# Kernel tuning notes

Measured on AMD Instinct MI355X. Metric: run time of the kernel, lower is better.

Reference implementation:

```python
import jax, jax.numpy as jnp
import numpy as np

B, S, D, H = 4, 2048, 1024, 16
HD = D // H


def setup_inputs() -> dict:
    key = jax.random.key(0)
    ks = jax.random.split(key, 9)
    s = 0.02  # GPT-2 init scale for weights
    return {
        "hidden_states": jax.random.normal(ks[0], (B, S, D), jnp.float32),
        "Wq": jax.random.normal(ks[1], (D, D), jnp.float32) * s,
        "bq": jnp.zeros((D,), jnp.float32),
        "Wk": jax.random.normal(ks[2], (D, D), jnp.float32) * s,
        "bk": jnp.zeros((D,), jnp.float32),
        "Wv": jax.random.normal(ks[3], (D, D), jnp.float32) * s,
        "bv": jnp.zeros((D,), jnp.float32),
        "Wo": jax.random.normal(ks[4], (D, D), jnp.float32) * s,
        "bo": jnp.zeros((D,), jnp.float32),
    }


def _split_heads(x):
    b, s, _ = x.shape
    return x.reshape(b, s, H, HD).transpose(0, 2, 1, 3)  # [B,H,S,HD]


def reference(hidden_states, Wq, bq, Wk, bk, Wv, bv, Wo, bo):
    b, s, d = hidden_states.shape
    q = _split_heads(hidden_states @ Wq + bq)
    k = _split_heads(hidden_states @ Wk + bk)
    v = _split_heads(hidden_states @ Wv + bv)
    # naive attention: full [B,H,S,S] scores, scale, causal where-mask, softmax, AV
    scores = jnp.einsum('bhqd,bhkd->bhqk', q, k)
    scores = scores / jnp.asarray(HD, scores.dtype) ** 0.5  # scale_attn_weights
    causal = jnp.tril(jnp.ones((s, s), dtype=bool))  # bias buffer slice
    scores = jnp.where(causal, scores, jnp.finfo(scores.dtype).min)
    attn = jax.nn.softmax(scores, axis=-1)  # attn_dropout p=0 -> identity
    out = jnp.einsum('bhqk,bhkd->bhqd', attn, v)
    out = out.transpose(0, 2, 1, 3).reshape(b, s, d)  # merge heads
    return out @ Wo + bo  # resid_dropout p=0 -> identity
```

## Files before the change

### kernel.cpp

```cpp
#include <hip/hip_runtime.h>
#include <stdint.h>


#define GAS __attribute__((address_space(1)))
#define LAS __attribute__((address_space(3)))

typedef __attribute__((ext_vector_type(4))) float f32x4;
typedef __attribute__((ext_vector_type(8))) short bf16x8;

__device__ __forceinline__ short f2bf(float f) {
  union { float f; uint32_t u; } v; v.f = f;
  uint32_t r = v.u + 0x7fffu + ((v.u >> 16) & 1u);
  return (short)(r >> 16);
}

__device__ __forceinline__ float bf2f(short s) {
  union { uint32_t u; float f; } v;
  v.u = ((uint32_t)(uint16_t)s) << 16;
  return v.f;
}

__device__ __forceinline__ uint32_t cvt_pk_bf16(float lo, float hi) {
  uint32_t r;
  asm("v_cvt_pk_bf16_f32 %0, %1, %2" : "=v"(r) : "v"(lo), "v"(hi));
  return r;
}

__device__ __forceinline__ void gload_lds16(const void* g, void* l) {
  __builtin_amdgcn_global_load_lds((const GAS void*)g, (LAS void*)l, 16, 0, 0);
}

#define GATE(N)                                            \
  __builtin_amdgcn_sched_barrier(0);                       \
  asm volatile("s_waitcnt vmcnt(" #N ")" ::: "memory");    \
  __builtin_amdgcn_s_barrier();                            \
  __builtin_amdgcn_sched_barrier(0);

#define BAR_LGKM                                           \
  __builtin_amdgcn_sched_barrier(0);                       \
  asm volatile("s_waitcnt lgkmcnt(0)" ::: "memory");       \
  __builtin_amdgcn_s_barrier();                            \
  __builtin_amdgcn_sched_barrier(0);

__global__ __launch_bounds__(256) void cvt_bf16_kernel(const float* __restrict__ in,
                                                       short* __restrict__ out, int n4) {
  int i = blockIdx.x * blockDim.x + threadIdx.x;
  int stride = gridDim.x * blockDim.x;
  for (int idx = i; idx < n4; idx += stride) {
    float4 v = ((const float4*)in)[idx];
    short4 o;
    o.x = f2bf(v.x); o.y = f2bf(v.y); o.z = f2bf(v.z); o.w = f2bf(v.w);
    ((short4*)out)[idx] = o;
  }
}

__global__ __launch_bounds__(256) void wt4_kernel(const float* __restrict__ W0,
                                                  const float* __restrict__ W1,
                                                  const float* __restrict__ W2,
                                                  const float* __restrict__ W3,
                                                  short* __restrict__ Wt) {
  __shared__ short tile[64][65];
  const float* W = (blockIdx.z == 0) ? W0 : (blockIdx.z == 1) ? W1
                   : (blockIdx.z == 2) ? W2 : W3;
  short* dst = Wt + ((size_t)blockIdx.z << 20);
  const int k0 = blockIdx.x * 64, n0 = blockIdx.y * 64;
  const int t = threadIdx.x;
#pragma unroll
  for (int i = 0; i < 16; ++i) {
    int r = (t >> 6) + i * 4, c = t & 63;
    tile[r][c] = f2bf(W[(size_t)(k0 + r) * 1024 + n0 + c]);
  }
  __syncthreads();
#pragma unroll
  for (int i = 0; i < 16; ++i) {
    int r = (t >> 6) + i * 4, c = t & 63;
    dst[(size_t)(n0 + r) * 1024 + k0 + c] = tile[c][r];
  }
}

template <int MODE>
__global__ __launch_bounds__(512, 2) void gemm2(const short* __restrict__ A,
                                                const short* __restrict__ Bt,
                                                const float* __restrict__ b0,
                                                const float* __restrict__ b1,
                                                const float* __restrict__ b2,
                                                void* __restrict__ O0,
                                                void* __restrict__ O1,
                                                void* __restrict__ O2) {
  __shared__ short lds[4][12288];
  const int xcd = (int)blockIdx.x & 7;
  const int t = (int)blockIdx.x >> 3;
  const int m0 = (xcd * 4 + (t & 3)) * 256;
  const int n0 = (t >> 2) * 128;
  const int tid = threadIdx.x;
  const int lane = tid & 63, w = tid >> 6;
  const int l15 = lane & 15, lg = lane >> 4;
  const int wm = w >> 1, wn = w & 1;

  const short* ag[2];
  const short* bg;
#pragma unroll
  for (int i = 0; i < 2; ++i) {
    const int P = w * 64 + i * 512 + lane;
    const int L = P ^ ((P >> 3) & 7);
    ag[i] = A + (size_t)(m0 + (L >> 2)) * 1024 + (L & 3) * 8;
  }
  {
    const int P = w * 64 + lane;
    const int L = P ^ ((P >> 3) & 7);
    bg = Bt + (size_t)(n0 + (L >> 2)) * 1024 + (L & 3) * 8;
  }

  int aof[4], bof[4];
#pragma unroll
  for (int mf = 0; mf < 4; ++mf) {
    const int L = (wm * 64 + mf * 16 + l15) * 4 + lg;
    aof[mf] = (L ^ ((L >> 3) & 7)) * 8;
  }
#pragma unroll
  for (int nf = 0; nf < 4; ++nf) {
    const int L = (wn * 64 + nf * 16 + l15) * 4 + lg;
    bof[nf] = (L ^ ((L >> 3) & 7)) * 8;
  }

  f32x4 acc[4][4];
#pragma unroll
  for (int i = 0; i < 4; ++i)
#pragma unroll
    for (int j = 0; j < 4; ++j) acc[i][j] = (f32x4){0.f, 0.f, 0.f, 0.f};

  auto stage = [&](int bi, int kt) {
    short* As = &lds[bi][0];
    short* Bs = &lds[bi][8192];
#pragma unroll
    for (int i = 0; i < 2; ++i)
      gload_lds16(ag[i] + kt * 32, As + (w * 64 + i * 512) * 8);
    gload_lds16(bg + kt * 32, Bs + (w * 64) * 8);
  };

  auto compute = [&](int bi) {
    const short* As = &lds[bi][0];
    const short* Bs = &lds[bi][8192];
    bf16x8 a[4], b[4];
#pragma unroll
    for (int mf = 0; mf < 4; ++mf) a[mf] = *(const bf16x8*)&As[aof[mf]];
#pragma unroll
    for (int nf = 0; nf < 4; ++nf) b[nf] = *(const bf16x8*)&Bs[bof[nf]];
    __builtin_amdgcn_s_setprio(1);
#pragma unroll
    for (int mf = 0; mf < 4; ++mf)
#pragma unroll
      for (int nf = 0; nf < 4; ++nf)
        acc[mf][nf] =
            __builtin_amdgcn_mfma_f32_16x16x32_bf16(a[mf], b[nf], acc[mf][nf], 0, 0, 0);
    __builtin_amdgcn_s_setprio(0);
  };

  stage(0, 0);
  stage(1, 1);
  stage(2, 2);

  for (int j = 0; j < 29; ++j) {
    GATE(6)
    stage((j + 3) & 3, j + 3);
    compute(j & 3);
  }
  GATE(6) compute(1);
  GATE(3) compute(2);
  GATE(0) compute(3);

  if (MODE == 1) {
    float* dst = (float*)O0;
#pragma unroll
    for (int mf = 0; mf < 4; ++mf)
#pragma unroll
      for (int nf = 0; nf < 4; ++nf) {
        const int col = n0 + wn * 64 + nf * 16 + l15;
        const float bv = b0[col];
#pragma unroll
        for (int rr = 0; rr < 4; ++rr) {
          const int row = m0 + wm * 64 + mf * 16 + lg * 4 + rr;
          dst[(size_t)row * 1024 + col] = acc[mf][nf][rr] + bv;
        }
      }
  } else {
    const int mat = n0 >> 10;
    const int nc0 = n0 & 1023;
    const float* bias = (mat == 0) ? b0 : (mat == 1) ? b1 : b2;
    if (mat < 2) {
      short* dst = (short*)(mat == 0 ? O0 : O1);
#pragma unroll
      for (int mf = 0; mf < 4; ++mf)
#pragma unroll
        for (int nf = 0; nf < 4; ++nf) {
          const int col = nc0 + wn * 64 + nf * 16 + l15;
          const float bv = bias[col];
          const int h = col >> 6, hd = col & 63;
#pragma unroll
          for (int rr = 0; rr < 4; ++rr) {
            const int row = m0 + wm * 64 + mf * 16 + lg * 4 + rr;
            const int b = row >> 11, s = row & 2047;
            dst[((size_t)(b * 16 + h) * 2048 + s) * 64 + hd] = f2bf(acc[mf][nf][rr] + bv);
          }
        }
    } else {
      short* dst = (short*)O2;
#pragma unroll
      for (int mf = 0; mf < 4; ++mf) {
        const int rowb = m0 + wm * 64 + mf * 16 + lg * 4;
        const int b = rowb >> 11, s = rowb & 2047;
#pragma unroll
        for (int nf = 0; nf < 4; ++nf) {
          const int col = nc0 + wn * 64 + nf * 16 + l15;
          const float bv = bias[col];
          const int h = col >> 6, hd = col & 63;
          short4 sv;
          sv.x = f2bf(acc[mf][nf][0] + bv);
          sv.y = f2bf(acc[mf][nf][1] + bv);
          sv.z = f2bf(acc[mf][nf][2] + bv);
          sv.w = f2bf(acc[mf][nf][3] + bv);
          *(short4*)&dst[((size_t)(b * 16 + h) * 64 + hd) * 2048 + s] = sv;
        }
      }
    }
  }
}

__global__ __launch_bounds__(256) void attn_kernel(const short* __restrict__ Q,
                                                   const short* __restrict__ K,
                                                   const short* __restrict__ Vt,
                                                   short* __restrict__ Oout) {
  __shared__ short Ks[2][4096];
  __shared__ short Vs[2][4096];
  const int bh = blockIdx.x;
  const int jq = 15 - (int)blockIdx.y;
  const int q0 = jq * 128;
  const int tid = threadIdx.x;
  const int lane = tid & 63, w = tid >> 6;
  const int l15 = lane & 15, lg = lane >> 4;
  const short* Qb = Q + (size_t)bh * 2048 * 64;
  const short* Kb = K + (size_t)bh * 2048 * 64;
  const short* Vb = Vt + (size_t)bh * 64 * 2048;
  const int b = bh >> 4, h = bh & 15;
  const float SC = 0.18033688011112042f;
  const int qg0 = q0 + w * 32;

  bf16x8 qf[2][2];
#pragma unroll
  for (int qs = 0; qs < 2; ++qs)
#pragma unroll
    for (int kk = 0; kk < 2; ++kk) {
      bf16x8 rq =
          *(const bf16x8*)&Qb[(size_t)(qg0 + qs * 16 + l15) * 64 + kk * 32 + lg * 8];
      union { uint32_t u[4]; bf16x8 v; } sq;
#pragma unroll
      for (int d = 0; d < 4; ++d)
        sq.u[d] = cvt_pk_bf16(bf2f(rq[2 * d]) * SC, bf2f(rq[2 * d + 1]) * SC);
      qf[qs][kk] = sq.v;
    }

  const short* kg[2];
  const short* vg[2];
#pragma unroll
  for (int i = 0; i < 2; ++i) {
    const int P = (w * 2 + i) * 64 + lane;
    const int L = P ^ ((P >> 3) & 7);
    kg[i] = Kb + (size_t)(L >> 3) * 64 + (L & 7) * 8;
    vg[i] = Vb + (size_t)(L >> 3) * 2048 + (L & 7) * 8;
  }

  int kcol[2], vca[2], vcb[2];
#pragma unroll
  for (int kk = 0; kk < 2; ++kk) {
    kcol[kk] = (((kk * 4 + lg) ^ (l15 & 7)) << 3);
    vca[kk] = (((kk * 4 + (lg >> 1)) ^ (l15 & 7)) << 3) + (lg & 1) * 4;
    vcb[kk] = (((kk * 4 + 2 + (lg >> 1)) ^ (l15 & 7)) << 3) + (lg & 1) * 4;
  }

  f32x4 o[2][4];
#pragma unroll
  for (int i = 0; i < 2; ++i)
#pragma unroll
    for (int j = 0; j < 4; ++j) o[i][j] = (f32x4){0.f, 0.f, 0.f, 0.f};
  f32x4 psum[2] = {(f32x4){0.f, 0.f, 0.f, 0.f}, (f32x4){0.f, 0.f, 0.f, 0.f}};

  const int nkt = 2 * jq + 2;
#pragma unroll
  for (int i = 0; i < 2; ++i) {
    gload_lds16(kg[i], &Ks[0][(w * 2 + i) * 512]);
    gload_lds16(vg[i], &Vs[0][(w * 2 + i) * 512]);
  }

  int cur = 0;
  for (int kt = 0; kt < nkt; ++kt) {
    if (kt + 1 < nkt) {
#pragma unroll
      for (int i = 0; i < 2; ++i) {
        gload_lds16(kg[i] + (kt + 1) * 4096, &Ks[cur ^ 1][(w * 2 + i) * 512]);
        gload_lds16(vg[i] + (kt + 1) * 64, &Vs[cur ^ 1][(w * 2 + i) * 512]);
      }
      GATE(4)
    } else {
      GATE(0)
    }

    if (kt * 64 <= qg0 + 31) {
      const short* Kc = &Ks[cur][0];
      const short* Vc = &Vs[cur][0];

      f32x4 sacc[4][2];
#pragma unroll
      for (int t = 0; t < 4; ++t)
#pragma unroll
        for (int qs = 0; qs < 2; ++qs) sacc[t][qs] = (f32x4){0.f, 0.f, 0.f, 0.f};
      __builtin_amdgcn_s_setprio(1);
#pragma unroll
      for (int t = 0; t < 4; ++t) {
        const int krow = (t * 16 + l15) * 64;
#pragma unroll
        for (int kk = 0; kk < 2; ++kk) {
          bf16x8 kf = *(const bf16x8*)&Kc[krow + kcol[kk]];
#pragma unroll
          for (int qs = 0; qs < 2; ++qs)
            sacc[t][qs] = __builtin_amdgcn_mfma_f32_16x16x32_bf16(kf, qf[qs][kk],
                                                                  sacc[t][qs], 0, 0, 0);
        }
      }
      __builtin_amdgcn_s_setprio(0);

      if (kt * 64 + 63 > qg0) {
#pragma unroll
        for (int t = 0; t < 4; ++t)
#pragma unroll
          for (int qs = 0; qs < 2; ++qs)
#pragma unroll
            for (int r = 0; r < 4; ++r) {
              const int kg_ = kt * 64 + t * 16 + lg * 4 + r;
              const int qg = qg0 + qs * 16 + l15;
              if (kg_ > qg) sacc[t][qs][r] = -3e38f;
            }
      }

      bf16x8 pa[2][2];
#pragma unroll
      for (int qs = 0; qs < 2; ++qs) {
#pragma unroll
        for (int t = 0; t < 4; ++t)
#pragma unroll
          for (int r = 0; r < 4; ++r) {
            const float p = __builtin_amdgcn_exp2f(sacc[t][qs][r]);
            sacc[t][qs][r] = p;
            psum[qs][r] += p;
          }
#pragma unroll
        for (int kk = 0; kk < 2; ++kk) {
          union { uint32_t u[4]; bf16x8 v; } pw;
          pw.u[0] = cvt_pk_bf16(sacc[2 * kk][qs][0], sacc[2 * kk][qs][1]);
          pw.u[1] = cvt_pk_bf16(sacc[2 * kk][qs][2], sacc[2 * kk][qs][3]);
          pw.u[2] = cvt_pk_bf16(sacc[2 * kk + 1][qs][0], sacc[2 * kk + 1][qs][1]);
          pw.u[3] = cvt_pk_bf16(sacc[2 * kk + 1][qs][2], sacc[2 * kk + 1][qs][3]);
          pa[qs][kk] = pw.v;
        }
      }

      __builtin_amdgcn_s_setprio(1);
#pragma unroll
      for (int ds = 0; ds < 4; ++ds) {
        const int vrow = (ds * 16 + l15) * 64;
#pragma unroll
        for (int kk = 0; kk < 2; ++kk) {
          union { short s[8]; bf16x8 v; short4 h2[2]; } vu;
          vu.h2[0] = *(const short4*)&Vc[vrow + vca[kk]];
          vu.h2[1] = *(const short4*)&Vc[vrow + vcb[kk]];
#pragma unroll
          for (int qs = 0; qs < 2; ++qs)
            o[qs][ds] = __builtin_amdgcn_mfma_f32_16x16x32_bf16(pa[qs][kk], vu.v,
                                                                o[qs][ds], 0, 0, 0);
        }
      }
      __builtin_amdgcn_s_setprio(0);
    }

    BAR_LGKM
    cur ^= 1;
  }

#pragma unroll
  for (int qs = 0; qs < 2; ++qs) {
    float s = psum[qs][0] + psum[qs][1] + psum[qs][2] + psum[qs][3];
    s += __shfl_xor(s, 16);
    s += __shfl_xor(s, 32);
    psum[qs][0] = 1.f / s;
  }

#pragma unroll
  for (int qs = 0; qs < 2; ++qs) {
    float on[4];
#pragma unroll
    for (int r = 0; r < 4; ++r)
      on[r] = __shfl(psum[qs][0], (lane & 48) | (lg * 4 + r));
#pragma unroll
    for (int ds = 0; ds < 4; ++ds)
#pragma unroll
      for (int r = 0; r < 4; ++r) {
        const int qg = q0 + w * 32 + qs * 16 + lg * 4 + r;
        const int col = h * 64 + ds * 16 + l15;
        Oout[((size_t)(b * 2048 + qg)) * 1024 + col] = f2bf(o[qs][ds][r] * on[r]);
      }
  }
}

extern "C" void kernel_launch(void* const* d_in, const int* in_sizes, int n_in,
                              void* d_out, int out_size, void* d_ws, size_t ws_size,
                              hipStream_t stream) {
  const float* hs = (const float*)d_in[0];
  const float* Wq = (const float*)d_in[1];
  const float* bq = (const float*)d_in[2];
  const float* Wk = (const float*)d_in[3];
  const float* bk = (const float*)d_in[4];
  const float* Wv = (const float*)d_in[5];
  const float* bv = (const float*)d_in[6];
  const float* Wo = (const float*)d_in[7];
  const float* bo = (const float*)d_in[8];

  char* ws = (char*)d_ws;
  short* Xbf = (short*)(ws + 0);
  short* Qb  = (short*)(ws + ((size_t)16 << 20));
  short* Kb  = (short*)(ws + ((size_t)32 << 20));
  short* Vtb = (short*)(ws + ((size_t)48 << 20));
  short* Wts = (short*)(ws + ((size_t)64 << 20));
  short* Wot = Wts + ((size_t)3 << 20);

  cvt_bf16_kernel<<<2048, 256, 0, stream>>>(hs, Xbf, (8192 * 1024) / 4);
  wt4_kernel<<<dim3(16, 16, 4), 256, 0, stream>>>(Wq, Wk, Wv, Wo, Wts);

  gemm2<0><<<768, 512, 0, stream>>>(Xbf, Wts, bq, bk, bv, Qb, Kb, Vtb);

  attn_kernel<<<dim3(64, 16), 256, 0, stream>>>(Qb, Kb, Vtb, Xbf);

  gemm2<1><<<256, 512, 0, stream>>>(Xbf, Wot, bo, nullptr, nullptr,
                                    (float*)d_out, nullptr, nullptr);
}
```

Baseline: 159.0 us.

## Triple-buffer KV in attention, permute V layout, compute row sums via MFMA

```diff
diff --git a/kernel.cpp b/kernel.cpp
--- a/kernel.cpp
+++ b/kernel.cpp
@@ -33,12 +33,6 @@
 #define GATE(N)                                            \
   __builtin_amdgcn_sched_barrier(0);                       \
   asm volatile("s_waitcnt vmcnt(" #N ")" ::: "memory");    \
-  __builtin_amdgcn_s_barrier();                            \
-  __builtin_amdgcn_sched_barrier(0);
-
-#define BAR_LGKM                                           \
-  __builtin_amdgcn_sched_barrier(0);                       \
-  asm volatile("s_waitcnt lgkmcnt(0)" ::: "memory");       \
   __builtin_amdgcn_s_barrier();                            \
   __builtin_amdgcn_sched_barrier(0);
 
@@ -209,6 +203,7 @@
       for (int mf = 0; mf < 4; ++mf) {
         const int rowb = m0 + wm * 64 + mf * 16 + lg * 4;
         const int b = rowb >> 11, s = rowb & 2047;
+        const int s2 = (s & ~31) | (((s >> 2) & 3) << 3) | (((s >> 4) & 1) << 2);
 #pragma unroll
         for (int nf = 0; nf < 4; ++nf) {
           const int col = nc0 + wn * 64 + nf * 16 + l15;
@@ -219,7 +214,7 @@
           sv.y = f2bf(acc[mf][nf][1] + bv);
           sv.z = f2bf(acc[mf][nf][2] + bv);
           sv.w = f2bf(acc[mf][nf][3] + bv);
-          *(short4*)&dst[((size_t)(b * 16 + h) * 64 + hd) * 2048 + s] = sv;
+          *(short4*)&dst[((size_t)(b * 16 + h) * 64 + hd) * 2048 + s2] = sv;
         }
       }
     }
@@ -230,10 +225,11 @@
                                                    const short* __restrict__ K,
                                                    const short* __restrict__ Vt,
                                                    short* __restrict__ Oout) {
-  __shared__ short Ks[2][4096];
-  __shared__ short Vs[2][4096];
-  const int bh = blockIdx.x;
-  const int jq = 15 - (int)blockIdx.y;
+  __shared__ short Ks[3][4096];
+  __shared__ short Vs[3][4096];
+  const int g = (int)blockIdx.x;
+  const int bh = (((g >> 3) & 7) << 3) | (g & 7);
+  const int jq = 15 - (g >> 6);
   const int q0 = jq * 128;
   const int tid = threadIdx.x;
   const int lane = tid & 63, w = tid >> 6;
@@ -259,6 +255,10 @@
       qf[qs][kk] = sq.v;
     }
 
+  union { short s[8]; bf16x8 v; } one_u;
+#pragma unroll
+  for (int i = 0; i < 8; ++i) one_u.s[i] = (short)0x3F80;
+
   const short* kg[2];
   const short* vg[2];
 #pragma unroll
@@ -269,12 +269,11 @@
     vg[i] = Vb + (size_t)(L >> 3) * 2048 + (L & 7) * 8;
   }
 
-  int kcol[2], vca[2], vcb[2];
+  int kcol[2], vcol[2];
 #pragma unroll
   for (int kk = 0; kk < 2; ++kk) {
     kcol[kk] = (((kk * 4 + lg) ^ (l15 & 7)) << 3);
-    vca[kk] = (((kk * 4 + (lg >> 1)) ^ (l15 & 7)) << 3) + (lg & 1) * 4;
-    vcb[kk] = (((kk * 4 + 2 + (lg >> 1)) ^ (l15 & 7)) << 3) + (lg & 1) * 4;
+    vcol[kk] = kcol[kk];
   }
 
   f32x4 o[2][4];
@@ -282,26 +281,30 @@
   for (int i = 0; i < 2; ++i)
 #pragma unroll
     for (int j = 0; j < 4; ++j) o[i][j] = (f32x4){0.f, 0.f, 0.f, 0.f};
-  f32x4 psum[2] = {(f32x4){0.f, 0.f, 0.f, 0.f}, (f32x4){0.f, 0.f, 0.f, 0.f}};
+  f32x4 psacc[2] = {(f32x4){0.f, 0.f, 0.f, 0.f}, (f32x4){0.f, 0.f, 0.f, 0.f}};
+
+  auto stageKV = [&](int bi, int kt) {
+#pragma unroll
+    for (int i = 0; i < 2; ++i) {
+      gload_lds16(kg[i] + (size_t)kt * 4096, &Ks[bi][(w * 2 + i) * 512]);
+      gload_lds16(vg[i] + kt * 64, &Vs[bi][(w * 2 + i) * 512]);
+    }
+  };
 
   const int nkt = 2 * jq + 2;
-#pragma unroll
-  for (int i = 0; i < 2; ++i) {
-    gload_lds16(kg[i], &Ks[0][(w * 2 + i) * 512]);
-    gload_lds16(vg[i], &Vs[0][(w * 2 + i) * 512]);
-  }
+  stageKV(0, 0);
+  stageKV(1, 1);
 
   int cur = 0;
   for (int kt = 0; kt < nkt; ++kt) {
     if (kt + 1 < nkt) {
-#pragma unroll
-      for (int i = 0; i < 2; ++i) {
-        gload_lds16(kg[i] + (kt + 1) * 4096, &Ks[cur ^ 1][(w * 2 + i) * 512]);
-        gload_lds16(vg[i] + (kt + 1) * 64, &Vs[cur ^ 1][(w * 2 + i) * 512]);
-      }
       GATE(4)
     } else {
       GATE(0)
+    }
+    if (kt + 2 < nkt) {
+      int nb = cur + 2; if (nb >= 3) nb -= 3;
+      stageKV(nb, kt + 2);
     }
 
     if (kt * 64 <= qg0 + 31) {
@@ -347,11 +350,8 @@
 #pragma unroll
         for (int t = 0; t < 4; ++t)
 #pragma unroll
-          for (int r = 0; r < 4; ++r) {
-            const float p = __builtin_amdgcn_exp2f(sacc[t][qs][r]);
-            sacc[t][qs][r] = p;
-            psum[qs][r] += p;
-          }
+          for (int r = 0; r < 4; ++r)
+            sacc[t][qs][r] = __builtin_amdgcn_exp2f(sacc[t][qs][r]);
 #pragma unroll
         for (int kk = 0; kk < 2; ++kk) {
           union { uint32_t u[4]; bf16x8 v; } pw;
@@ -369,43 +369,37 @@
         const int vrow = (ds * 16 + l15) * 64;
 #pragma unroll
         for (int kk = 0; kk < 2; ++kk) {
-          union { short s[8]; bf16x8 v; short4 h2[2]; } vu;
-          vu.h2[0] = *(const short4*)&Vc[vrow + vca[kk]];
-          vu.h2[1] = *(const short4*)&Vc[vrow + vcb[kk]];
+          bf16x8 vf = *(const bf16x8*)&Vc[vrow + vcol[kk]];
 #pragma unroll
           for (int qs = 0; qs < 2; ++qs)
-            o[qs][ds] = __builtin_amdgcn_mfma_f32_16x16x32_bf16(pa[qs][kk], vu.v,
+            o[qs][ds] = __builtin_amdgcn_mfma_f32_16x16x32_bf16(pa[qs][kk], vf,
                                                                 o[qs][ds], 0, 0, 0);
         }
       }
+#pragma unroll
+      for (int qs = 0; qs < 2; ++qs)
+#pragma unroll
+        for (int kk = 0; kk < 2; ++kk)
+          psacc[qs] = __builtin_amdgcn_mfma_f32_16x16x32_bf16(pa[qs][kk], one_u.v,
+                                                              psacc[qs], 0, 0, 0);
       __builtin_amdgcn_s_setprio(0);
     }
 
-    BAR_LGKM
-    cur ^= 1;
+    cur = cur + 1 == 3 ? 0 : cur + 1;
   }
 
 #pragma unroll
   for (int qs = 0; qs < 2; ++qs) {
-    float s = psum[qs][0] + psum[qs][1] + psum[qs][2] + psum[qs][3];
-    s += __shfl_xor(s, 16);
-    s += __shfl_xor(s, 32);
-    psum[qs][0] = 1.f / s;
-  }
-
-#pragma unroll
-  for (int qs = 0; qs < 2; ++qs) {
-    float on[4];
-#pragma unroll
-    for (int r = 0; r < 4; ++r)
-      on[r] = __shfl(psum[qs][0], (lane & 48) | (lg * 4 + r));
+    float inv[4];
+#pragma unroll
+    for (int r = 0; r < 4; ++r) inv[r] = 1.f / psacc[qs][r];
 #pragma unroll
     for (int ds = 0; ds < 4; ++ds)
 #pragma unroll
       for (int r = 0; r < 4; ++r) {
         const int qg = q0 + w * 32 + qs * 16 + lg * 4 + r;
         const int col = h * 64 + ds * 16 + l15;
-        Oout[((size_t)(b * 2048 + qg)) * 1024 + col] = f2bf(o[qs][ds][r] * on[r]);
+        Oout[((size_t)(b * 2048 + qg)) * 1024 + col] = f2bf(o[qs][ds][r] * inv[r]);
       }
   }
 }
@@ -436,7 +430,7 @@
 
   gemm2<0><<<768, 512, 0, stream>>>(Xbf, Wts, bq, bk, bv, Qb, Kb, Vtb);
 
-  attn_kernel<<<dim3(64, 16), 256, 0, stream>>>(Qb, Kb, Vtb, Xbf);
+  attn_kernel<<<1024, 256, 0, stream>>>(Qb, Kb, Vtb, Xbf);
 
   gemm2<1><<<256, 512, 0, stream>>>(Xbf, Wot, bo, nullptr, nullptr,
                                     (float*)d_out, nullptr, nullptr);
```

Measured after the change: 152.0 us. -4.4%, faster.
